# Optimization experiments

Hardware: AMD Instinct MI355X
Metric: run time of the kernel (lower is better)

The kernel has to match this reference:

```python
import jax, jax.numpy as jnp
import numpy as np

EPS = 1e-5
AVG_D = 32.0


def setup_inputs() -> dict:
    key = jax.random.key(0)
    ks = jax.random.split(key, 12)
    Ns, Nd, E, D, K = 1_000_000, 100_000, 3_200_000, 16, 2
    Fs, Fd, V = 4, 4, 100_000
    F = Fd + K  # predictor fields
    inp = {}
    inp["Cat_src"] = jax.random.randint(ks[0], (Ns, Fs), 0, V)
    inp["Cat_dst"] = jax.random.randint(ks[1], (Nd, Fd), 0, V)
    inp["src_ids"] = jax.random.randint(ks[2], (E,), 0, Ns)
    inp["dst_ids"] = jax.random.randint(ks[3], (E,), 0, Nd)
    inp["label"] = jax.random.randint(ks[4], (Nd,), 0, 2)
    inp["w"] = jax.random.normal(ks[5], (V, D), dtype=jnp.float32) * 0.05
    inp["W_agg"] = jax.random.normal(ks[6], (K, 12 * D, D), dtype=jnp.float32) * 0.05
    inp["b_agg"] = jnp.zeros((K, D), jnp.float32)
    inp["w_lin"] = jax.random.normal(ks[7], (F * D,), dtype=jnp.float32) * 0.05
    inp["b_lin"] = jnp.zeros((1,), jnp.float32)
    inp["W1"] = jax.random.normal(ks[8], (F * D, 64), dtype=jnp.float32) * 0.05
    inp["b1"] = jnp.zeros((64,), jnp.float32)
    inp["W2"] = jax.random.normal(ks[9], (64, 32), dtype=jnp.float32) * 0.05
    inp["b2"] = jnp.zeros((32,), jnp.float32)
    inp["W3"] = jax.random.normal(ks[10], (32, 1), dtype=jnp.float32) * 0.05
    inp["b3"] = jnp.zeros((1,), jnp.float32)
    return inp


def reference(Cat_src, Cat_dst, src_ids, dst_ids, label, w, W_agg, b_agg,
              w_lin, b_lin, W1, b1, W2, b2, W3, b3):
    Nd = Cat_dst.shape[0]
    # --- node embedding: gather cat fields, RowEmb with modes [mean, max] -> [Ns, K, D]
    emb = w[Cat_src]                                      # [Ns, Fs, D]
    h_src = jnp.stack([emb.mean(1), emb.max(1)], axis=1)  # [Ns, K, D]
    # --- multi-aggregator message passing (copy_u + segment min/max/mean, std via mean of h^2)
    m = h_src[src_ids]                                    # [E, K, D]
    deg = jax.ops.segment_sum(jnp.ones(src_ids.shape, m.dtype), dst_ids, Nd)
    safe = jnp.maximum(deg, 1.0)[:, None, None]
    mean = jax.ops.segment_sum(m, dst_ids, Nd) / safe
    mean2 = jax.ops.segment_sum(m * m, dst_ids, Nd) / safe
    has = (deg > 0)[:, None, None]
    mn = jnp.where(has, jax.ops.segment_min(m, dst_ids, Nd), 0.0)
    mx = jnp.where(has, jax.ops.segment_max(m, dst_ids, Nd), 0.0)
    std = jnp.sqrt(jax.nn.relu(mean2 - mean * mean) + EPS)
    tmp = jnp.concatenate([mean, mn, mx, std], axis=-1)   # [Nd, K, 4D]
    # --- PNA degree scalers: identity / amplification / attenuation
    logd = jnp.log(deg + 1.0)
    log_avg = jnp.log(AVG_D + 1.0)
    amp = (logd / log_avg)[:, None, None]
    att = jnp.where(logd > 0, log_avg / jnp.maximum(logd, EPS), 0.0)[:, None, None]
    scaled = jnp.concatenate([tmp, tmp * amp, tmp * att], axis=-1)  # [Nd, K, 12D]
    mes = jnp.einsum('nkf,kfd->nkd', scaled, W_agg) + b_agg          # [Nd, K, D]
    # --- final block: concat dst cat embeddings with aggregated messages
    x = jnp.concatenate([w[Cat_dst], mes], axis=1)        # [Nd, F, D]
    # --- DeepFM predictor: linear + FM pairwise + deep MLP
    flat = x.reshape(Nd, -1)
    lin = flat @ w_lin + b_lin[0]
    s = x.sum(1)
    fm = 0.5 * ((s * s) - (x * x).sum(1)).sum(-1)
    h = jax.nn.relu(flat @ W1 + b1)
    h = jax.nn.relu(h @ W2 + b2)
    deep = (h @ W3 + b3)[:, 0]
    pred = jax.nn.sigmoid(lin + fm + deep)
    return (pred, label)
```

## Files before the change

### kernel.cpp

```cpp
#include <hip/hip_runtime.h>
#include <math.h>

#define EPSF 1e-5f
#define BSH  5
#define BSZ  32
#define MAXB 4096
#define SBH  9
#define MAXSB 256
#define TILE 4096
#define BCAP 1472
#define XPAD 100
#define X2PADS 72
#define HISTB 512

typedef __attribute__((ext_vector_type(8))) short short8;
typedef __attribute__((ext_vector_type(4))) float float4v;

__device__ inline unsigned f2bf_rne(float x) {
    unsigned u = __float_as_uint(x);
    u += 0x7FFF + ((u >> 16) & 1);
    return u >> 16;
}
__device__ inline short bf16_of(float x) { return (short)f2bf_rne(x); }
__device__ inline float bf2f_lo(unsigned hv) { return __uint_as_float(hv << 16); }
__device__ inline float bf2f_hi(unsigned hv) { return __uint_as_float(hv & 0xFFFF0000u); }
__device__ inline float bf2f_s(ushort s) { return __uint_as_float((unsigned)s << 16); }

__global__ void cast_w(const float* __restrict__ w, ushort* __restrict__ wb, int n) {
    int i4 = (blockIdx.x * 256 + threadIdx.x) * 4;
    if (i4 + 3 < n) {
        float4 v = *(const float4*)(w + i4);
        ushort4 o;
        o.x = (ushort)f2bf_rne(v.x); o.y = (ushort)f2bf_rne(v.y);
        o.z = (ushort)f2bf_rne(v.z); o.w = (ushort)f2bf_rne(v.w);
        *(ushort4*)(wb + i4) = o;
    } else {
        for (int j = i4; j < n; ++j) wb[j] = (ushort)f2bf_rne(w[j]);
    }
}

__global__ __launch_bounds__(256) void build_h_hist(
    const int* __restrict__ Cat_src, const float* __restrict__ w,
    unsigned* __restrict__ h, int Ns,
    const int* __restrict__ dst_ids, int* bcount, int E, int nb)
{
    __shared__ int hsh[MAXB];
    if (blockIdx.x < HISTB) {
        for (int i = threadIdx.x; i < nb; i += 256) hsh[i] = 0;
        __syncthreads();
        int stride = HISTB * 256;
        for (int e = blockIdx.x * 256 + threadIdx.x; e < E; e += stride)
            atomicAdd(&hsh[dst_ids[e] >> BSH], 1);
        __syncthreads();
        for (int i = threadIdx.x; i < nb; i += 256) {
            int c = hsh[i];
            if (c) atomicAdd(&bcount[i], c);
        }
        return;
    }
    int gid = (blockIdx.x - HISTB) * 256 + threadIdx.x;
    int s = gid >> 4;
    if (s >= Ns) return;
    int lane = threadIdx.x & 63;
    int d = lane & 15;
    int c = Cat_src[s * 4 + (d & 3)];
    float vs = 0.f, vm = -INFINITY;
#pragma unroll
    for (int f = 0; f < 4; ++f) {
        int id = __shfl(c, (lane & 48) + f, 64);
        float a = w[id * 16 + d];
        vs += a; vm = fmaxf(vm, a);
    }
    unsigned packed = f2bf_rne(vs * 0.25f) | (f2bf_rne(vm) << 16);
    __builtin_nontemporal_store(packed, &h[s * 16 + d]);
}

__global__ void zero_bcount(int* bcount, int nb) {
    int i = blockIdx.x * 256 + threadIdx.x;
    if (i < nb) bcount[i] = 0;
}

__global__ __launch_bounds__(256) void scan_buckets(const int* __restrict__ bcount,
                                                    int* bstart, int* sbcursor, int nb) {
    __shared__ int lsum[256];
    int tid = threadIdx.x;
    int v[16];
    int s = 0;
#pragma unroll
    for (int j = 0; j < 16; ++j) {
        int idx = tid * 16 + j;
        v[j] = (idx < nb) ? bcount[idx] : 0;
        s += v[j];
    }
    lsum[tid] = s;
    __syncthreads();
    for (int off = 1; off < 256; off <<= 1) {
        int y = (tid >= off) ? lsum[tid - off] : 0;
        __syncthreads();
        lsum[tid] += y;
        __syncthreads();
    }
    int run = lsum[tid] - s;
    if (tid * 16 < nb) sbcursor[tid] = run;
#pragma unroll
    for (int j = 0; j < 16; ++j) {
        int idx = tid * 16 + j;
        if (idx < nb) bstart[idx] = run;
        run += v[j];
    }
}

__global__ __launch_bounds__(256) void scatter_sb(
    const int* __restrict__ src_ids, const int* __restrict__ dst_ids,
    int* sbcursor, unsigned* __restrict__ pairs1, int E, int nsb)
{
    __shared__ int cnt[MAXSB];
    __shared__ int base[MAXSB];
    int tid = threadIdx.x;
    int t0 = blockIdx.x * TILE;
    for (int i = tid; i < nsb; i += 256) cnt[i] = 0;
    __syncthreads();
    int rank[TILE / 256];
#pragma unroll
    for (int j = 0; j < TILE / 256; ++j) {
        int e = t0 + j * 256 + tid;
        rank[j] = (e < E) ? atomicAdd(&cnt[dst_ids[e] >> SBH], 1) : 0;
    }
    __syncthreads();
    for (int i = tid; i < nsb; i += 256) {
        int c = cnt[i];
        base[i] = c ? atomicAdd(&sbcursor[i], c) : 0;
    }
    __syncthreads();
#pragma unroll
    for (int j = 0; j < TILE / 256; ++j) {
        int e = t0 + j * 256 + tid;
        if (e < E) {
            int d = dst_ids[e];
            int sb = d >> SBH;
            pairs1[base[sb] + rank[j]] =
                ((unsigned)src_ids[e] << 9) | (unsigned)(d & 511);
        }
    }
}

__global__ __launch_bounds__(256) void scatter_fine(
    const unsigned* __restrict__ pairs1, const int* __restrict__ bstart,
    unsigned* __restrict__ pairs2, int nb, int nsb, int E)
{
    __shared__ int cur[16];
    int S = blockIdx.x, tid = threadIdx.x;
    int sbs = bstart[S << 4];
    int sbe = (S == nsb - 1) ? E : bstart[(S + 1) << 4];
    if (tid < 16) {
        int idx = (S << 4) + tid;
        cur[tid] = (idx < nb) ? bstart[idx] : 0;
    }
    __syncthreads();
    for (int i = sbs + tid; i < sbe; i += 256) {
        unsigned p = __builtin_nontemporal_load(&pairs1[i]);
        int fb = (p >> 5) & 15;
        int pos = atomicAdd(&cur[fb], 1);
        pairs2[pos] = p;
    }
}


__device__ inline void bucket_sort(const unsigned* __restrict__ pairs,
                                   int gbase, int cnt,
                                   unsigned* sp, int* hist, int* ofs, int* start,
                                   int tid)
{
    if (tid < BSZ) hist[tid] = 0;
    __syncthreads();
    for (int i = tid; i < cnt; i += 256)
        atomicAdd(&hist[__builtin_nontemporal_load(&pairs[gbase + i]) & (BSZ - 1)], 1);
    __syncthreads();
    if (tid < BSZ) ofs[tid] = hist[tid];
    __syncthreads();
    for (int off = 1; off < BSZ; off <<= 1) {
        int y = (tid < BSZ && tid >= off) ? ofs[tid - off] : 0;
        __syncthreads();
        if (tid < BSZ) ofs[tid] += y;
        __syncthreads();
    }
    if (tid < BSZ) {
        start[tid] = ofs[tid] - hist[tid];
        ofs[tid] = ofs[tid] - hist[tid];
    }
    __syncthreads();
    for (int i = tid; i < cnt; i += 256) {
        unsigned p = __builtin_nontemporal_load(&pairs[gbase + i]);
        int r = atomicAdd(&ofs[p & (BSZ - 1)], 1);
        sp[r] = p;
    }
    __syncthreads();
}

__device__ inline void emit_stats(float sum0, float sq0, float mn0, float mx0,
                                  float sum1, float sq1, float mn1, float mx1,
                                  int dg, int n, int lane, int sub,
                                  ushort* __restrict__ tmpb, int* __restrict__ deg_out)
{
#pragma unroll
    for (int off = 16; off <= 32; off <<= 1) {
        sum0 += __shfl_xor(sum0, off); sq0 += __shfl_xor(sq0, off);
        mn0 = fminf(mn0, __shfl_xor(mn0, off)); mx0 = fmaxf(mx0, __shfl_xor(mx0, off));
        sum1 += __shfl_xor(sum1, off); sq1 += __shfl_xor(sq1, off);
        mn1 = fminf(mn1, __shfl_xor(mn1, off)); mx1 = fmaxf(mx1, __shfl_xor(mx1, off));
    }
    float safe = fmaxf((float)dg, 1.f);
    float r = 1.f / safe;
    bool has = dg > 0;
    float mean0 = sum0 * r, mean1 = sum1 * r;
    float sd0 = sqrtf(fmaxf(sq0 * r - mean0 * mean0, 0.f) + EPSF);
    float sd1 = sqrtf(fmaxf(sq1 * r - mean1 * mean1, 0.f) + EPSF);
    float v0 = (sub == 0) ? mean0 : (sub == 1) ? (has ? mn0 : 0.f)
             : (sub == 2) ? (has ? mx0 : 0.f) : sd0;
    float v1 = (sub == 0) ? mean1 : (sub == 1) ? (has ? mn1 : 0.f)
             : (sub == 2) ? (has ? mx1 : 0.f) : sd1;
    ushort* tp = tmpb + (size_t)n * 128;
    tp[lane] = (ushort)f2bf_rne(v0);
    tp[64 + lane] = (ushort)f2bf_rne(v1);
    if (lane == 0) deg_out[n] = dg;
}

__global__ __launch_bounds__(256) void agg_from_h(
    const unsigned* __restrict__ h,
    const int* __restrict__ bstart, const int* __restrict__ bcount,
    const unsigned* __restrict__ pairs,
    ushort* __restrict__ tmpb, int* __restrict__ deg_out, int Nd)
{
    __shared__ unsigned sp[BCAP];
    __shared__ int hist[BSZ];
    __shared__ int ofs[BSZ];
    __shared__ int start[BSZ];
    int b = blockIdx.x, tid = threadIdx.x;
    int cnt = bcount[b];
    int gbase = bstart[b];
    if (cnt > BCAP) cnt = BCAP;
    bucket_sort(pairs, gbase, cnt, sp, hist, ofs, start, tid);

    int wv = tid >> 6, lane = tid & 63, sub = lane >> 4, d = lane & 15;
#pragma unroll 1
    for (int q = 0; q < 8; ++q) {
        int dl = wv * 8 + q;
        int n = b * BSZ + dl;
        if (n >= Nd) break;
        int st = start[dl], dg = hist[dl];
        float sum0 = 0.f, sq0 = 0.f, mn0 = INFINITY, mx0 = -INFINITY;
        float sum1 = 0.f, sq1 = 0.f, mn1 = INFINITY, mx1 = -INFINITY;
        int nt = (dg + 15) >> 4;
        for (int t = 0; t < nt; ++t) {
            int base = t * 16 + sub;
            unsigned hv[4];
#pragma unroll
            for (int j = 0; j < 4; ++j) {
                int e = base + j * 4;
                int ec = (e < dg) ? e : (dg - 1);
                unsigned p = sp[st + ec];
                hv[j] = h[(p >> 9) * 16 + d];
            }
#pragma unroll
            for (int j = 0; j < 4; ++j) {
                int e = base + j * 4;
                if (e < dg) {
                    float me = bf2f_lo(hv[j]);
                    float vm = bf2f_hi(hv[j]);
                    sum0 += me; sq0 += me * me;
                    mn0 = fminf(mn0, me); mx0 = fmaxf(mx0, me);
                    sum1 += vm; sq1 += vm * vm;
                    mn1 = fminf(mn1, vm); mx1 = fmaxf(mx1, vm);
                }
            }
        }
        emit_stats(sum0, sq0, mn0, mx0, sum1, sq1, mn1, mx1,
                   dg, n, lane, sub, tmpb, deg_out);
    }
}

__global__ __launch_bounds__(256) void agg_from_w(
    const int* __restrict__ Cat_src, const float* __restrict__ w,
    const ushort* __restrict__ wb, int use_bf,
    const int* __restrict__ bstart, const int* __restrict__ bcount,
    const unsigned* __restrict__ pairs,
    ushort* __restrict__ tmpb, int* __restrict__ deg_out, int Nd)
{
    __shared__ unsigned sp[BCAP];
    __shared__ int hist[BSZ];
    __shared__ int ofs[BSZ];
    __shared__ int start[BSZ];
    int b = blockIdx.x, tid = threadIdx.x;
    int cnt = bcount[b];
    int gbase = bstart[b];
    if (cnt > BCAP) cnt = BCAP;
    bucket_sort(pairs, gbase, cnt, sp, hist, ofs, start, tid);

    int wv = tid >> 6, lane = tid & 63, sub = lane >> 4, d = lane & 15;
#pragma unroll 1
    for (int q = 0; q < 8; ++q) {
        int dl = wv * 8 + q;
        int n = b * BSZ + dl;
        if (n >= Nd) break;
        int st = start[dl], dg = hist[dl];
        float sum0 = 0.f, sq0 = 0.f, mn0 = INFINITY, mx0 = -INFINITY;
        float sum1 = 0.f, sq1 = 0.f, mn1 = INFINITY, mx1 = -INFINITY;
        int nt = (dg + 3) >> 2;
        for (int t = 0; t < nt; ++t) {
            int e4 = t * 4 + sub;
            int ec = (e4 < dg) ? e4 : (dg - 1);
            unsigned p = sp[st + ec];
            int src = (int)(p >> 9);
            int cat = Cat_src[src * 4 + (d & 3)];
            float vs = 0.f, vm = -INFINITY;
            if (use_bf) {
#pragma unroll
                for (int f = 0; f < 4; ++f) {
                    int id = __shfl(cat, sub * 16 + f, 64);
                    float a = bf2f_s(wb[id * 16 + d]);
                    vs += a; vm = fmaxf(vm, a);
                }
            } else {
#pragma unroll
                for (int f = 0; f < 4; ++f) {
                    int id = __shfl(cat, sub * 16 + f, 64);
                    float a = w[id * 16 + d];
                    vs += a; vm = fmaxf(vm, a);
                }
            }
            if (e4 < dg) {
                float me = vs * 0.25f;
                sum0 += me; sq0 += me * me;
                mn0 = fminf(mn0, me); mx0 = fmaxf(mx0, me);
                sum1 += vm; sq1 += vm * vm;
                mn1 = fminf(mn1, vm); mx1 = fmaxf(mx1, vm);
            }
        }
        emit_stats(sum0, sq0, mn0, mx0, sum1, sq1, mn1, mx1,
                   dg, n, lane, sub, tmpb, deg_out);
    }
}

__global__ __launch_bounds__(256) void finalize_mfma(
    const int* __restrict__ Cat_dst, const int* __restrict__ label,
    const float* __restrict__ w,
    const float* __restrict__ W_agg, const float* __restrict__ b_agg,
    const float* __restrict__ w_lin, const float* __restrict__ b_lin,
    const float* __restrict__ W1, const float* __restrict__ b1,
    const float* __restrict__ W2, const float* __restrict__ b2,
    const float* __restrict__ W3, const float* __restrict__ b3,
    const int* __restrict__ deg_arr, const ushort* __restrict__ tmpb,
    float* __restrict__ out, int Nd)
{
    __shared__ __align__(16) float sx[4][16 * XPAD];
    __shared__ __align__(16) ushort sx2[4][16 * X2PADS];
    __shared__ float sdeep[4][16];

    int tid = threadIdx.x;
    int wv = tid >> 6, lane = tid & 63;
    int q = lane >> 4, m = lane & 15;
    int n0 = (blockIdx.x * 4 + wv) * 16;
    int n = n0 + m;
    int nc = (n < Nd) ? n : (Nd - 1);

    float* X = sx[wv];
    ushort* X2 = sx2[wv];

    float fdeg = (float)deg_arr[nc];
    float logd = logf(fdeg + 1.f);
    const float logavg = logf(33.0f);
    float amp = logd / logavg;
    float att = (logd > 0.f) ? (logavg / fmaxf(logd, EPSF)) : 0.f;
    float ampr[4], attr[4];
#pragma unroll
    for (int r = 0; r < 4; ++r) {
        ampr[r] = __shfl(amp, q * 4 + r, 64);
        attr[r] = __shfl(att, q * 4 + r, 64);
    }

    const ushort* tpn = tmpb + (size_t)nc * 128;
#pragma unroll
    for (int kvar = 0; kvar < 2; ++kvar) {
        short8 af0 = *(const short8*)(tpn + kvar * 64 + q * 8);
        short8 af1 = *(const short8*)(tpn + kvar * 64 + 32 + q * 8);
        const float* WB = W_agg + kvar * 3072;
        float4v aI = {0.f,0.f,0.f,0.f}, aA = {0.f,0.f,0.f,0.f}, aT = {0.f,0.f,0.f,0.f};
#pragma unroll
        for (int sb = 0; sb < 3; ++sb) {
            short8 b0, b1v;
            const float* bp0 = WB + (sb * 64 + q * 8) * 16 + m;
            const float* bp1 = WB + (sb * 64 + 32 + q * 8) * 16 + m;
#pragma unroll
            for (int j = 0; j < 8; ++j) {
                b0[j]  = bf16_of(bp0[j * 16]);
                b1v[j] = bf16_of(bp1[j * 16]);
            }
            if (sb == 0) {
                aI = __builtin_amdgcn_mfma_f32_16x16x32_bf16(af0, b0, aI, 0, 0, 0);
                aI = __builtin_amdgcn_mfma_f32_16x16x32_bf16(af1, b1v, aI, 0, 0, 0);
            } else if (sb == 1) {
                aA = __builtin_amdgcn_mfma_f32_16x16x32_bf16(af0, b0, aA, 0, 0, 0);
                aA = __builtin_amdgcn_mfma_f32_16x16x32_bf16(af1, b1v, aA, 0, 0, 0);
            } else {
                aT = __builtin_amdgcn_mfma_f32_16x16x32_bf16(af0, b0, aT, 0, 0, 0);
                aT = __builtin_amdgcn_mfma_f32_16x16x32_bf16(af1, b1v, aT, 0, 0, 0);
            }
        }
        float bias = b_agg[kvar * 16 + m];
#pragma unroll
        for (int r = 0; r < 4; ++r)
            X[(q * 4 + r) * XPAD + 64 + kvar * 16 + m] =
                aI[r] + ampr[r] * aA[r] + attr[r] * aT[r] + bias;
    }

    {
        int nl = lane >> 2, fl = lane & 3;
        int nn = n0 + nl;
        int nnc = (nn < Nd) ? nn : (Nd - 1);
        int cid = Cat_dst[nnc * 4 + fl];
        const float4* R = (const float4*)(w + (size_t)cid * 16);
        float* xp = X + nl * XPAD + fl * 16;
        *(float4*)(xp + 0)  = R[0];
        *(float4*)(xp + 4)  = R[1];
        *(float4*)(xp + 8)  = R[2];
        *(float4*)(xp + 12) = R[3];
    }
    __syncthreads();

    float lin = 0.f, sq = 0.f;
    float sd[16];
#pragma unroll
    for (int u = 0; u < 16; ++u) sd[u] = 0.f;
    {
        const float* xp = X + m * XPAD + q * 16;
        const float* wl = w_lin + q * 16;
#pragma unroll
        for (int u = 0; u < 16; ++u) {
            float v = xp[u];
            lin += v * wl[u]; sq += v * v; sd[u] += v;
        }
    }
    if (q < 2) {
        const float* xp = X + m * XPAD + (4 + q) * 16;
        const float* wl = w_lin + (4 + q) * 16;
#pragma unroll
        for (int u = 0; u < 16; ++u) {
            float v = xp[u];
            lin += v * wl[u]; sq += v * v; sd[u] += v;
        }
    }
#pragma unroll
    for (int off = 16; off <= 32; off <<= 1) {
        lin += __shfl_xor(lin, off);
        sq  += __shfl_xor(sq, off);
#pragma unroll
        for (int u = 0; u < 16; ++u) sd[u] += __shfl_xor(sd[u], off);
    }
    float fm = 0.f;
#pragma unroll
    for (int u = 0; u < 16; ++u) fm += sd[u] * sd[u];
    fm = 0.5f * (fm - sq);

    short8 xa[3];
#pragma unroll
    for (int t = 0; t < 3; ++t) {
        const float* xp = X + m * XPAD + t * 32 + q * 8;
        float4 a0 = *(const float4*)xp;
        float4 a1 = *(const float4*)(xp + 4);
        xa[t][0] = bf16_of(a0.x); xa[t][1] = bf16_of(a0.y);
        xa[t][2] = bf16_of(a0.z); xa[t][3] = bf16_of(a0.w);
        xa[t][4] = bf16_of(a1.x); xa[t][5] = bf16_of(a1.y);
        xa[t][6] = bf16_of(a1.z); xa[t][7] = bf16_of(a1.w);
    }
#pragma unroll
    for (int nt = 0; nt < 4; ++nt) {
        float4v acc = {0.f, 0.f, 0.f, 0.f};
#pragma unroll
        for (int t = 0; t < 3; ++t) {
            const float* bp = W1 + (t * 32 + q * 8) * 64 + nt * 16 + m;
            short8 bf;
#pragma unroll
            for (int j = 0; j < 8; ++j) bf[j] = bf16_of(bp[j * 64]);
            acc = __builtin_amdgcn_mfma_f32_16x16x32_bf16(xa[t], bf, acc, 0, 0, 0);
        }
        float bb = b1[nt * 16 + m];
#pragma unroll
        for (int r = 0; r < 4; ++r)
            X2[(q * 4 + r) * X2PADS + nt * 16 + m] =
                (ushort)f2bf_rne(fmaxf(acc[r] + bb, 0.f));
    }
    __syncthreads();

    short8 ha[2];
#pragma unroll
    for (int t = 0; t < 2; ++t)
        ha[t] = *(const short8*)(X2 + m * X2PADS + t * 32 + q * 8);
    float dp[4] = {0.f, 0.f, 0.f, 0.f};
#pragma unroll
    for (int nt = 0; nt < 2; ++nt) {
        float4v acc = {0.f, 0.f, 0.f, 0.f};
#pragma unroll
        for (int t = 0; t < 2; ++t) {
            const float* bp = W2 + (t * 32 + q * 8) * 32 + nt * 16 + m;
            short8 bf;
#pragma unroll
            for (int j = 0; j < 8; ++j) bf[j] = bf16_of(bp[j * 32]);
            acc = __builtin_amdgcn_mfma_f32_16x16x32_bf16(ha[t], bf, acc, 0, 0, 0);
        }
        float bb = b2[nt * 16 + m];
        float w3 = W3[nt * 16 + m];
#pragma unroll
        for (int r = 0; r < 4; ++r)
            dp[r] += fmaxf(acc[r] + bb, 0.f) * w3;
    }
#pragma unroll
    for (int off = 1; off <= 8; off <<= 1) {
#pragma unroll
        for (int r = 0; r < 4; ++r) dp[r] += __shfl_xor(dp[r], off);
    }
    if (m < 4)
        sdeep[wv][q * 4 + m] = (m == 0) ? dp[0] : (m == 1) ? dp[1]
                             : (m == 2) ? dp[2] : dp[3];
    __syncthreads();
    float deep = sdeep[wv][m];

    if (q == 0 && n < Nd) {
        float z = lin + b_lin[0] + fm + deep + b3[0];
        float pred = 1.f / (1.f + expf(-z));
        out[n] = pred;
        out[Nd + n] = (float)label[n];
    }
}

extern "C" void kernel_launch(void* const* d_in, const int* in_sizes, int n_in,
                              void* d_out, int out_size, void* d_ws, size_t ws_size,
                              hipStream_t stream) {
    const int*   Cat_src = (const int*)d_in[0];
    const int*   Cat_dst = (const int*)d_in[1];
    const int*   src_ids = (const int*)d_in[2];
    const int*   dst_ids = (const int*)d_in[3];
    const int*   label   = (const int*)d_in[4];
    const float* w       = (const float*)d_in[5];
    const float* W_agg   = (const float*)d_in[6];
    const float* b_agg   = (const float*)d_in[7];
    const float* w_lin   = (const float*)d_in[8];
    const float* b_lin   = (const float*)d_in[9];
    const float* W1      = (const float*)d_in[10];
    const float* b1      = (const float*)d_in[11];
    const float* W2      = (const float*)d_in[12];
    const float* b2      = (const float*)d_in[13];
    const float* W3      = (const float*)d_in[14];
    const float* b3      = (const float*)d_in[15];

    int E  = in_sizes[2];
    int Nd = in_sizes[4];
    int Ns = in_sizes[0] / 4;
    int VD = in_sizes[5];
    int nb  = (Nd + BSZ - 1) >> BSH;
    int nsb = (nb + 15) >> 4;

    int* bcount   = (int*)d_ws;
    int* bstart   = bcount + MAXB;
    int* sbcursor = bstart + MAXB;
    int* deg      = sbcursor + MAXSB;
    unsigned* pairs1 = (unsigned*)(deg + Nd);
    unsigned* pairs2 = pairs1 + E;
    size_t off_tmp = (((size_t)(MAXB * 2 + MAXSB + Nd) + 2 * (size_t)E) * 4 + 255)
                     & ~(size_t)255;
    ushort* tmpb = (ushort*)((char*)d_ws + off_tmp);
    ushort* w_bf16 = tmpb + (size_t)Nd * 128;
    unsigned* h  = (unsigned*)(w_bf16 + VD);

    size_t need_common = off_tmp + (size_t)Nd * 256;
    size_t need_A = need_common + (size_t)VD * 2;
    size_t need_B = need_A + (size_t)Ns * 64;
    int mode = (ws_size >= need_B) ? 2 : (ws_size >= need_A) ? 1 : 0;

    float* out = (float*)d_out;

    hipLaunchKernelGGL(zero_bcount, dim3((nb + 255) / 256), dim3(256), 0, stream,
                       bcount, nb);
    if (mode == 2) {
        int hb = (int)(((size_t)Ns * 16 + 255) / 256);
        hipLaunchKernelGGL(build_h_hist, dim3(HISTB + hb), dim3(256), 0, stream,
                           Cat_src, w, h, Ns, dst_ids, bcount, E, nb);
    } else {
        hipLaunchKernelGGL(build_h_hist, dim3(HISTB), dim3(256), 0, stream,
                           Cat_src, w, h, 0, dst_ids, bcount, E, nb);
    }
    hipLaunchKernelGGL(scan_buckets, dim3(1), dim3(256), 0, stream,
                       bcount, bstart, sbcursor, nb);
    hipLaunchKernelGGL(scatter_sb, dim3((E + TILE - 1) / TILE), dim3(256), 0, stream,
                       src_ids, dst_ids, sbcursor, pairs1, E, nsb);
    hipLaunchKernelGGL(scatter_fine, dim3(nsb), dim3(256), 0, stream,
                       pairs1, bstart, pairs2, nb, nsb, E);
    if (mode == 2) {
        hipLaunchKernelGGL(agg_from_h, dim3(nb), dim3(256), 0, stream,
                           h, bstart, bcount, pairs2, tmpb, deg, Nd);
    } else {
        if (mode == 1)
            hipLaunchKernelGGL(cast_w, dim3((VD / 4 + 255) / 256), dim3(256),
                               0, stream, w, w_bf16, VD);
        hipLaunchKernelGGL(agg_from_w, dim3(nb), dim3(256), 0, stream,
                           Cat_src, w, w_bf16, mode, bstart, bcount, pairs2,
                           tmpb, deg, Nd);
    }
    hipLaunchKernelGGL(finalize_mfma, dim3((Nd + 63) / 64), dim3(256), 0, stream,
                       Cat_dst, label, w, W_agg, b_agg, w_lin, b_lin,
                       W1, b1, W2, b2, W3, b3, deg, tmpb, out, Nd);
}
```

Before: 346.0 us.

## Fuse aggregation and DeepFM finalize into one kernel for the h path

After: 364.6 us. +5.4%, slower.

```diff
diff --git a/kernel.cpp b/kernel.cpp
--- a/kernel.cpp
+++ b/kernel.cpp
@@ -11,6 +11,7 @@
 #define BCAP 1472
 #define XPAD 100
 #define X2PADS 72
+#define STATP 136
 #define HISTB 512
 
 typedef __attribute__((ext_vector_type(8))) short short8;
@@ -197,6 +198,272 @@
     __syncthreads();
 }
 
+__global__ __launch_bounds__(256) void agg_fin_h(
+    const unsigned* __restrict__ h,
+    const int* __restrict__ bstart, const int* __restrict__ bcount,
+    const unsigned* __restrict__ pairs,
+    const int* __restrict__ Cat_dst, const int* __restrict__ label,
+    const float* __restrict__ w,
+    const float* __restrict__ W_agg, const float* __restrict__ b_agg,
+    const float* __restrict__ w_lin, const float* __restrict__ b_lin,
+    const float* __restrict__ W1, const float* __restrict__ b1,
+    const float* __restrict__ W2, const float* __restrict__ b2,
+    const float* __restrict__ W3, const float* __restrict__ b3,
+    float* __restrict__ out, int Nd)
+{
+    __shared__ unsigned sp[BCAP];
+    __shared__ int hist[BSZ];
+    __shared__ int ofs[BSZ];
+    __shared__ int start[BSZ];
+    __shared__ __align__(16) ushort stat[BSZ * STATP];
+    __shared__ __align__(16) float sx[2][16 * XPAD];
+    __shared__ __align__(16) ushort sx2[2][16 * X2PADS];
+    __shared__ float sdeep[2][16];
+
+    int b = blockIdx.x, tid = threadIdx.x;
+    int cnt = bcount[b];
+    int gbase = bstart[b];
+    if (cnt > BCAP) cnt = BCAP;
+    bucket_sort(pairs, gbase, cnt, sp, hist, ofs, start, tid);
+
+    int wv = tid >> 6, lane = tid & 63, sub = lane >> 4, d = lane & 15;
+#pragma unroll 1
+    for (int q = 0; q < 8; ++q) {
+        int dl = wv * 8 + q;
+        int n = b * BSZ + dl;
+        if (n >= Nd) break;
+        int st = start[dl], dg = hist[dl];
+        float sum0 = 0.f, sq0 = 0.f, mn0 = INFINITY, mx0 = -INFINITY;
+        float sum1 = 0.f, sq1 = 0.f, mn1 = INFINITY, mx1 = -INFINITY;
+        int nt = (dg + 15) >> 4;
+        for (int t = 0; t < nt; ++t) {
+            int base = t * 16 + sub;
+            unsigned hv[4];
+#pragma unroll
+            for (int j = 0; j < 4; ++j) {
+                int e = base + j * 4;
+                int ec = (e < dg) ? e : (dg - 1);
+                unsigned p = sp[st + ec];
+                hv[j] = h[(p >> 9) * 16 + d];
+            }
+#pragma unroll
+            for (int j = 0; j < 4; ++j) {
+                int e = base + j * 4;
+                if (e < dg) {
+                    float me = bf2f_lo(hv[j]);
+                    float vm = bf2f_hi(hv[j]);
+                    sum0 += me; sq0 += me * me;
+                    mn0 = fminf(mn0, me); mx0 = fmaxf(mx0, me);
+                    sum1 += vm; sq1 += vm * vm;
+                    mn1 = fminf(mn1, vm); mx1 = fmaxf(mx1, vm);
+                }
+            }
+        }
+#pragma unroll
+        for (int off = 16; off <= 32; off <<= 1) {
+            sum0 += __shfl_xor(sum0, off); sq0 += __shfl_xor(sq0, off);
+            mn0 = fminf(mn0, __shfl_xor(mn0, off)); mx0 = fmaxf(mx0, __shfl_xor(mx0, off));
+            sum1 += __shfl_xor(sum1, off); sq1 += __shfl_xor(sq1, off);
+            mn1 = fminf(mn1, __shfl_xor(mn1, off)); mx1 = fmaxf(mx1, __shfl_xor(mx1, off));
+        }
+        float safe = fmaxf((float)dg, 1.f);
+        float r = 1.f / safe;
+        bool has = dg > 0;
+        float mean0 = sum0 * r, mean1 = sum1 * r;
+        float sd0 = sqrtf(fmaxf(sq0 * r - mean0 * mean0, 0.f) + EPSF);
+        float sd1 = sqrtf(fmaxf(sq1 * r - mean1 * mean1, 0.f) + EPSF);
+        float v0 = (sub == 0) ? mean0 : (sub == 1) ? (has ? mn0 : 0.f)
+                 : (sub == 2) ? (has ? mx0 : 0.f) : sd0;
+        float v1 = (sub == 0) ? mean1 : (sub == 1) ? (has ? mn1 : 0.f)
+                 : (sub == 2) ? (has ? mx1 : 0.f) : sd1;
+        ushort* tp = stat + dl * STATP;
+        tp[lane] = (ushort)f2bf_rne(v0);
+        tp[64 + lane] = (ushort)f2bf_rne(v1);
+    }
+    __syncthreads();
+
+    int q = lane >> 4, m = lane & 15;
+    int n0 = b * BSZ + wv * 16;
+    int n = n0 + m;
+    int nc = (n < Nd) ? n : (Nd - 1);
+    bool fin = (wv < 2);
+
+    float* X = sx[wv & 1];
+    ushort* X2 = sx2[wv & 1];
+
+    if (fin) {
+        int dl = wv * 16 + m;
+        float fdeg = (float)hist[dl];
+        float logd = logf(fdeg + 1.f);
+        const float logavg = logf(33.0f);
+        float amp = logd / logavg;
+        float att = (logd > 0.f) ? (logavg / fmaxf(logd, EPSF)) : 0.f;
+        float ampr[4], attr[4];
+#pragma unroll
+        for (int r = 0; r < 4; ++r) {
+            ampr[r] = __shfl(amp, q * 4 + r, 64);
+            attr[r] = __shfl(att, q * 4 + r, 64);
+        }
+
+        const ushort* tpn = stat + (wv * 16 + m) * STATP;
+#pragma unroll
+        for (int kvar = 0; kvar < 2; ++kvar) {
+            short8 af0 = *(const short8*)(tpn + kvar * 64 + q * 8);
+            short8 af1 = *(const short8*)(tpn + kvar * 64 + 32 + q * 8);
+            const float* WB = W_agg + kvar * 3072;
+            float4v aI = {0.f,0.f,0.f,0.f}, aA = {0.f,0.f,0.f,0.f}, aT = {0.f,0.f,0.f,0.f};
+#pragma unroll
+            for (int sb = 0; sb < 3; ++sb) {
+                short8 b0, b1v;
+                const float* bp0 = WB + (sb * 64 + q * 8) * 16 + m;
+                const float* bp1 = WB + (sb * 64 + 32 + q * 8) * 16 + m;
+#pragma unroll
+                for (int j = 0; j < 8; ++j) {
+                    b0[j]  = bf16_of(bp0[j * 16]);
+                    b1v[j] = bf16_of(bp1[j * 16]);
+                }
+                if (sb == 0) {
+                    aI = __builtin_amdgcn_mfma_f32_16x16x32_bf16(af0, b0, aI, 0, 0, 0);
+                    aI = __builtin_amdgcn_mfma_f32_16x16x32_bf16(af1, b1v, aI, 0, 0, 0);
+                } else if (sb == 1) {
+                    aA = __builtin_amdgcn_mfma_f32_16x16x32_bf16(af0, b0, aA, 0, 0, 0);
+                    aA = __builtin_amdgcn_mfma_f32_16x16x32_bf16(af1, b1v, aA, 0, 0, 0);
+                } else {
+                    aT = __builtin_amdgcn_mfma_f32_16x16x32_bf16(af0, b0, aT, 0, 0, 0);
+                    aT = __builtin_amdgcn_mfma_f32_16x16x32_bf16(af1, b1v, aT, 0, 0, 0);
+                }
+            }
+            float bias = b_agg[kvar * 16 + m];
+#pragma unroll
+            for (int r = 0; r < 4; ++r)
+                X[(q * 4 + r) * XPAD + 64 + kvar * 16 + m] =
+                    aI[r] + ampr[r] * aA[r] + attr[r] * aT[r] + bias;
+        }
+
+        {
+            int nl = lane >> 2, fl = lane & 3;
+            int nn = n0 + nl;
+            int nnc = (nn < Nd) ? nn : (Nd - 1);
+            int cid = Cat_dst[nnc * 4 + fl];
+            const float4* R = (const float4*)(w + (size_t)cid * 16);
+            float* xp = X + nl * XPAD + fl * 16;
+            *(float4*)(xp + 0)  = R[0];
+            *(float4*)(xp + 4)  = R[1];
+            *(float4*)(xp + 8)  = R[2];
+            *(float4*)(xp + 12) = R[3];
+        }
+    }
+    __syncthreads();
+
+    float lin = 0.f, fm = 0.f;
+    short8 xa[3];
+    if (fin) {
+        float sq = 0.f;
+        float sd[16];
+#pragma unroll
+        for (int u = 0; u < 16; ++u) sd[u] = 0.f;
+        {
+            const float* xp = X + m * XPAD + q * 16;
+            const float* wl = w_lin + q * 16;
+#pragma unroll
+            for (int u = 0; u < 16; ++u) {
+                float v = xp[u];
+                lin += v * wl[u]; sq += v * v; sd[u] += v;
+            }
+        }
+        if (q < 2) {
+            const float* xp = X + m * XPAD + (4 + q) * 16;
+            const float* wl = w_lin + (4 + q) * 16;
+#pragma unroll
+            for (int u = 0; u < 16; ++u) {
+                float v = xp[u];
+                lin += v * wl[u]; sq += v * v; sd[u] += v;
+            }
+        }
+#pragma unroll
+        for (int off = 16; off <= 32; off <<= 1) {
+            lin += __shfl_xor(lin, off);
+            sq  += __shfl_xor(sq, off);
+#pragma unroll
+            for (int u = 0; u < 16; ++u) sd[u] += __shfl_xor(sd[u], off);
+        }
+#pragma unroll
+        for (int u = 0; u < 16; ++u) fm += sd[u] * sd[u];
+        fm = 0.5f * (fm - sq);
+
+#pragma unroll
+        for (int t = 0; t < 3; ++t) {
+            const float* xp = X + m * XPAD + t * 32 + q * 8;
+            float4 a0 = *(const float4*)xp;
+            float4 a1 = *(const float4*)(xp + 4);
+            xa[t][0] = bf16_of(a0.x); xa[t][1] = bf16_of(a0.y);
+            xa[t][2] = bf16_of(a0.z); xa[t][3] = bf16_of(a0.w);
+            xa[t][4] = bf16_of(a1.x); xa[t][5] = bf16_of(a1.y);
+            xa[t][6] = bf16_of(a1.z); xa[t][7] = bf16_of(a1.w);
+        }
+#pragma unroll
+        for (int nt = 0; nt < 4; ++nt) {
+            float4v acc = {0.f, 0.f, 0.f, 0.f};
+#pragma unroll
+            for (int t = 0; t < 3; ++t) {
+                const float* bp = W1 + (t * 32 + q * 8) * 64 + nt * 16 + m;
+                short8 bf;
+#pragma unroll
+                for (int j = 0; j < 8; ++j) bf[j] = bf16_of(bp[j * 64]);
+                acc = __builtin_amdgcn_mfma_f32_16x16x32_bf16(xa[t], bf, acc, 0, 0, 0);
+            }
+            float bb = b1[nt * 16 + m];
+#pragma unroll
+            for (int r = 0; r < 4; ++r)
+                X2[(q * 4 + r) * X2PADS + nt * 16 + m] =
+                    (ushort)f2bf_rne(fmaxf(acc[r] + bb, 0.f));
+        }
+    }
+    __syncthreads();
+
+    if (fin) {
+        short8 ha[2];
+#pragma unroll
+        for (int t = 0; t < 2; ++t)
+            ha[t] = *(const short8*)(X2 + m * X2PADS + t * 32 + q * 8);
+        float dp[4] = {0.f, 0.f, 0.f, 0.f};
+#pragma unroll
+        for (int nt = 0; nt < 2; ++nt) {
+            float4v acc = {0.f, 0.f, 0.f, 0.f};
+#pragma unroll
+            for (int t = 0; t < 2; ++t) {
+                const float* bp = W2 + (t * 32 + q * 8) * 32 + nt * 16 + m;
+                short8 bf;
+#pragma unroll
+                for (int j = 0; j < 8; ++j) bf[j] = bf16_of(bp[j * 32]);
+                acc = __builtin_amdgcn_mfma_f32_16x16x32_bf16(ha[t], bf, acc, 0, 0, 0);
+            }
+            float bb = b2[nt * 16 + m];
+            float w3 = W3[nt * 16 + m];
+#pragma unroll
+            for (int r = 0; r < 4; ++r)
+                dp[r] += fmaxf(acc[r] + bb, 0.f) * w3;
+        }
+#pragma unroll
+        for (int off = 1; off <= 8; off <<= 1) {
+#pragma unroll
+            for (int r = 0; r < 4; ++r) dp[r] += __shfl_xor(dp[r], off);
+        }
+        if (m < 4)
+            sdeep[wv][q * 4 + m] = (m == 0) ? dp[0] : (m == 1) ? dp[1]
+                                 : (m == 2) ? dp[2] : dp[3];
+    }
+    __syncthreads();
+
+    if (fin && q == 0 && n < Nd) {
+        float deep = sdeep[wv][m];
+        float z = lin + b_lin[0] + fm + deep + b3[0];
+        float pred = 1.f / (1.f + expf(-z));
+        out[n] = pred;
+        out[Nd + n] = (float)label[n];
+    }
+}
+
 __device__ inline void emit_stats(float sum0, float sq0, float mn0, float mx0,
                                   float sum1, float sq1, float mn1, float mx1,
                                   int dg, int n, int lane, int sub,
@@ -223,60 +490,6 @@
     tp[lane] = (ushort)f2bf_rne(v0);
     tp[64 + lane] = (ushort)f2bf_rne(v1);
     if (lane == 0) deg_out[n] = dg;
-}
-
-__global__ __launch_bounds__(256) void agg_from_h(
-    const unsigned* __restrict__ h,
-    const int* __restrict__ bstart, const int* __restrict__ bcount,
-    const unsigned* __restrict__ pairs,
-    ushort* __restrict__ tmpb, int* __restrict__ deg_out, int Nd)
-{
-    __shared__ unsigned sp[BCAP];
-    __shared__ int hist[BSZ];
-    __shared__ int ofs[BSZ];
-    __shared__ int start[BSZ];
-    int b = blockIdx.x, tid = threadIdx.x;
-    int cnt = bcount[b];
-    int gbase = bstart[b];
-    if (cnt > BCAP) cnt = BCAP;
-    bucket_sort(pairs, gbase, cnt, sp, hist, ofs, start, tid);
-
-    int wv = tid >> 6, lane = tid & 63, sub = lane >> 4, d = lane & 15;
-#pragma unroll 1
-    for (int q = 0; q < 8; ++q) {
-        int dl = wv * 8 + q;
-        int n = b * BSZ + dl;
-        if (n >= Nd) break;
-        int st = start[dl], dg = hist[dl];
-        float sum0 = 0.f, sq0 = 0.f, mn0 = INFINITY, mx0 = -INFINITY;
-        float sum1 = 0.f, sq1 = 0.f, mn1 = INFINITY, mx1 = -INFINITY;
-        int nt = (dg + 15) >> 4;
-        for (int t = 0; t < nt; ++t) {
-            int base = t * 16 + sub;
-            unsigned hv[4];
-#pragma unroll
-            for (int j = 0; j < 4; ++j) {
-                int e = base + j * 4;
-                int ec = (e < dg) ? e : (dg - 1);
-                unsigned p = sp[st + ec];
-                hv[j] = h[(p >> 9) * 16 + d];
-            }
-#pragma unroll
-            for (int j = 0; j < 4; ++j) {
-                int e = base + j * 4;
-                if (e < dg) {
-                    float me = bf2f_lo(hv[j]);
-                    float vm = bf2f_hi(hv[j]);
-                    sum0 += me; sq0 += me * me;
-                    mn0 = fminf(mn0, me); mx0 = fmaxf(mx0, me);
-                    sum1 += vm; sq1 += vm * vm;
-                    mn1 = fminf(mn1, vm); mx1 = fmaxf(mx1, vm);
-                }
-            }
-        }
-        emit_stats(sum0, sq0, mn0, mx0, sum1, sq1, mn1, mx1,
-                   dg, n, lane, sub, tmpb, deg_out);
-    }
 }
 
 __global__ __launch_bounds__(256) void agg_from_w(
@@ -412,7 +625,6 @@
             X[(q * 4 + r) * XPAD + 64 + kvar * 16 + m] =
                 aI[r] + ampr[r] * aA[r] + attr[r] * aT[r] + bias;
     }
-
     {
         int nl = lane >> 2, fl = lane & 3;
         int nn = n0 + nl;
@@ -595,8 +807,10 @@
     hipLaunchKernelGGL(scatter_fine, dim3(nsb), dim3(256), 0, stream,
                        pairs1, bstart, pairs2, nb, nsb, E);
     if (mode == 2) {
-        hipLaunchKernelGGL(agg_from_h, dim3(nb), dim3(256), 0, stream,
-                           h, bstart, bcount, pairs2, tmpb, deg, Nd);
+        hipLaunchKernelGGL(agg_fin_h, dim3(nb), dim3(256), 0, stream,
+                           h, bstart, bcount, pairs2,
+                           Cat_dst, label, w, W_agg, b_agg, w_lin, b_lin,
+                           W1, b1, W2, b2, W3, b3, out, Nd);
     } else {
         if (mode == 1)
             hipLaunchKernelGGL(cast_w, dim3((VD / 4 + 255) / 256), dim3(256),
@@ -604,8 +818,8 @@
         hipLaunchKernelGGL(agg_from_w, dim3(nb), dim3(256), 0, stream,
                            Cat_src, w, w_bf16, mode, bstart, bcount, pairs2,
                            tmpb, deg, Nd);
-    }
-    hipLaunchKernelGGL(finalize_mfma, dim3((Nd + 63) / 64), dim3(256), 0, stream,
-                       Cat_dst, label, w, W_agg, b_agg, w_lin, b_lin,
-                       W1, b1, W2, b2, W3, b3, deg, tmpb, out, Nd);
-}
+        hipLaunchKernelGGL(finalize_mfma, dim3((Nd + 63) / 64), dim3(256), 0, stream,
+                           Cat_dst, label, w, W_agg, b_agg, w_lin, b_lin,
+                           W1, b1, W2, b2, W3, b3, deg, tmpb, out, Nd);
+    }
+}
```
